# Kernel tuning notes

Measured on AMD Instinct MI355X. Metric: run time of the kernel, lower is better.

## Reference

```python
import math
from functools import partial

import jax
import jax.numpy as jnp
import numpy as np

DS = 128            # domain_size (cells per side); original used 600
PD = 1.0            # particle diameter d == grid spacing
KN = 500000.0       # normal stiffness
MASS = 1.0
DT = 1e-4
FS = 5              # filter (stencil) size -> 5x5x5 shifts
_ALPHA = -math.log(0.7) / math.pi
_GAMMA = _ALPHA / math.sqrt(_ALPHA ** 2 + 1.0)
ETA = 2.0 * _GAMMA * math.sqrt(KN * MASS)   # damping_coefficient_Eta
EPS = 1e-4          # torch.clamp(dist, 0.0001)
SHAPE = (1, 1, DS, DS, DS)


def setup_inputs() -> dict:
    rng = np.random.default_rng(0)
    occ = np.zeros((DS, DS, DS), np.float32)
    occ[1:-1, 1:-1, 1:-1] = (rng.random((DS - 2,) * 3) < 0.2).astype(np.float32)
    iz, iy, ix = np.meshgrid(np.arange(DS), np.arange(DS), np.arange(DS), indexing="ij")
    jit = lambda: (rng.random((DS,) * 3).astype(np.float32) - 0.5) * 0.4
    # occupied cells store their own coordinate (+jitter) so round(x/d) == cell index
    x = (occ * (ix.astype(np.float32) + jit())).astype(np.float32)
    y = (occ * (iy.astype(np.float32) + jit())).astype(np.float32)
    z = (occ * (iz.astype(np.float32) + jit())).astype(np.float32)
    vel = lambda: (occ * rng.normal(0.0, 0.5, (DS,) * 3)).astype(np.float32)
    asg = lambda a: jnp.asarray(a.reshape(SHAPE))
    return {
        "x_grid": asg(x), "y_grid": asg(y), "z_grid": asg(z),
        "vx_grid": asg(vel()), "vy_grid": asg(vel()), "vz_grid": asg(vel()),
        "mask": asg(occ),
    }


def _contrib(xg, yg, zg, vxg, vyg, vzg, shift):
    """Force contribution from one (i,j,k) stencil shift (torch.roll based)."""
    roll = lambda g: jnp.roll(g, shift, axis=(2, 3, 4))
    dx, dy, dz = xg - roll(xg), yg - roll(yg), zg - roll(zg)
    sq = dx * dx + dy * dy + dz * dz
    dist = jnp.sqrt(sq + 1e-20)  # tiny eps keeps sqrt grad finite at sq==0; value unchanged in fp32
    cd = jnp.maximum(dist, EPS)  # torch.clamp(dist, 0.0001)
    vn = ((vxg - roll(vxg)) * dx + (vyg - roll(vyg)) * dy + (vzg - roll(vzg)) * dz) / cd
    ov = dist < 2.0 * PD
    fx = jnp.where(ov, KN * (dist - 2.0 * PD) * dx / cd + ETA * vn * dx / cd, 0.0)
    fy = jnp.where(ov, KN * (dist - 2.0 * PD) * dy / cd + ETA * vn * dy / cd, 0.0)
    fz = jnp.where(ov, KN * (dist - 2.0 * PD) * dz / cd + ETA * vn * dz / cd, 0.0)
    return fx, fy, fz


def _forward(xg, yg, zg, vxg, vyg, vzg, mask):
    f32 = jnp.float32
    fx = jnp.zeros(SHAPE, f32)
    fy = jnp.zeros(SHAPE, f32)
    fz = jnp.zeros(SHAPE, f32)
    for i in range(FS):
        for j in range(FS):
            for k in range(FS):
                c = jax.checkpoint(partial(_contrib, shift=(k - 2, j - 2, i - 2)))
                dfx, dfy, dfz = c(xg, yg, zg, vxg, vyg, vzg)
                fx, fy, fz = fx + dfx, fy + dfy, fz + dfz
    # boundary overlap forces
    bl = ((xg != 0.0) & (xg < PD)).astype(f32)
    br = (xg > DS - 2.0 * PD).astype(f32)
    bb = ((yg != 0.0) & (yg < PD)).astype(f32)
    bt = (yg > DS - 2.0 * PD).astype(f32)
    bf = ((zg != 0.0) & (zg < PD)).astype(f32)
    bk = (zg > DS - 2.0 * PD).astype(f32)
    fxb = KN * bl * mask * (PD - xg) - KN * br * mask * (xg - DS + 2.0 * PD) - ETA * vxg * bl * mask - ETA * vxg * br * mask
    fyb = KN * bb * mask * (PD - yg) - KN * bt * mask * (yg - DS + 2.0 * PD) - ETA * vyg * bb * mask - ETA * vyg * bt * mask
    fzb = KN * bf * mask * (PD - zg) - KN * bk * mask * (zg - DS + 2.0 * PD) - ETA * vzg * bf * mask - ETA * vzg * bk * mask
    vxn = vxg + DT / MASS * mask * (-0.0 * MASS - fx + fxb)
    vyn = vyg + DT / MASS * mask * (-9.8 * MASS - fy + fyb)
    vzn = vzg + DT / MASS * mask * (-0.0 * MASS - fz + fzb)
    cell = lambda g: jnp.round(g / PD).astype(jnp.int32)
    cx0, cy0, cz0 = cell(xg), cell(yg), cell(zg)
    xn, yn, zn = xg + DT * vxn, yg + DT * vyn, zg + DT * vzn
    cx1, cy1, cz1 = cell(xn), cell(yn), cell(zn)
    # cell-list relocation: flatten to linear indices; invalid (empty) cells -> dump slot D3
    D3 = DS ** 3
    def lin(cz, cy, cx):
        v = (cx != 0) & (cy != 0) & (cz != 0)   # torch filters cell_* != 0
        return jnp.where(v, (cz * DS + cy) * DS + cx, D3).reshape(-1)
    lo = lin(cz0, cy0, cx0)
    ln = lin(cz1, cy1, cx1)
    pad = lambda g: jnp.concatenate([g.reshape(-1), jnp.zeros((1,), g.dtype)])
    unpad = lambda f: f[:D3].reshape(SHAPE)
    def move(g):
        gf = pad(g)
        return unpad(gf.at[lo].set(0.0).at[ln].set(gf[lo]))
    mask_n = unpad(pad(mask).at[lo].set(0.0).at[ln].set(1.0))
    return (move(xn), move(yn), move(zn), move(vxn), move(vyn), move(vzn), mask_n)


def reference(x_grid, y_grid, z_grid, vx_grid, vy_grid, vz_grid, mask):
    return _forward(x_grid, y_grid, z_grid, vx_grid, vy_grid, vz_grid, mask)
```

## Files before the change

### kernel.cpp

```cpp
#include <hip/hip_runtime.h>

#define DSZ   128
#define DMSK  127
#define D3    (DSZ * DSZ * DSZ)

#define KN_F   500000.0f
#define ETA_F  159.535258f
#define DT_F   1e-4f

#define TBX   32
#define TBY   4
#define TBZ   4
#define HALO  2
#define RS    37
#define PS    296
#define SLOTS 2368
#define NT    512

#define Q512  512.0f
#define IQ512 0.001953125f

struct OffTabs { int a[36]; int b[48]; int e[44]; };
constexpr OffTabs make_tabs() {
    OffTabs t{}; int na = 0, nb = 0, ne = 0;
    for (int dz = -2; dz <= 2; ++dz)
        for (int dy = -2; dy <= 2; ++dy)
            for (int dx = -2; dx <= 2; ++dx) {
                const int r2 = dz*dz + dy*dy + dx*dx;
                const int off = dz * PS + dy * RS + dx;
                if (r2 <= 4)      t.a[na++] = off;
                else if (r2 <= 6) t.b[nb++] = off;
                else              t.e[ne++] = off;
            }
    while (na < 36) t.a[na++] = 0;
    return t;
}
__constant__ OffTabs g_tabs = make_tabs();

typedef float f4a4 __attribute__((ext_vector_type(4), aligned(4)));

__device__ __forceinline__ unsigned q16(float x) {
    return (unsigned)(int)rintf(x * Q512);
}
__device__ __forceinline__ unsigned bf16_rne(float f) {
    unsigned u = __float_as_uint(f);
    u += 0x7fffu + ((u >> 16) & 1u);
    return u >> 16;
}
__device__ __forceinline__ float unpk_lo(unsigned w) { return __uint_as_float(w << 16); }
__device__ __forceinline__ float unpk_hi(unsigned w) { return __uint_as_float(w & 0xffff0000u); }

__device__ __forceinline__ void pair_full(
    const unsigned* __restrict__ lab, const unsigned* __restrict__ lcd,
    const unsigned* __restrict__ lvv, int n,
    float px, float py, float pz, float vx, float vy, float vz,
    float& fx, float& fy, float& fz)
{
    const unsigned ab = lab[n], cd = lcd[n];
    const float ddx = fmaf((float)(ab & 0xffffu), -IQ512, px);
    const float ddy = fmaf((float)(ab >> 16),     -IQ512, py);
    const float ddz = fmaf((float)(cd & 0xffffu), -IQ512, pz);
    const float sq  = fmaf(ddx, ddx, fmaf(ddy, ddy, fmaf(ddz, ddz, 1e-20f)));
    const float rsd = __builtin_amdgcn_rsqf(sq);
    const float dist = sq * rsd;
    const unsigned w = lvv[n];
    const float dvx = vx - __uint_as_float(cd & 0xffff0000u);
    const float dvy = vy - unpk_lo(w);
    const float dvz = vz - unpk_hi(w);
    const float vn = fmaf(dvx, ddx, fmaf(dvy, ddy, dvz * ddz)) * rsd;
    float coef = fmaf(KN_F, dist - 2.0f, ETA_F * vn) * rsd;
    coef = (dist < 2.0f) ? coef : 0.0f;
    fx = fmaf(coef, ddx, fx);
    fy = fmaf(coef, ddy, fy);
    fz = fmaf(coef, ddz, fz);
}

__global__ __launch_bounds__(NT) void dem_tile(
    const float* __restrict__ X, const float* __restrict__ Y, const float* __restrict__ Z,
    const float* __restrict__ VX, const float* __restrict__ VY, const float* __restrict__ VZ,
    float* __restrict__ out)
{
    __shared__ unsigned lsbuf[3 * SLOTS];
    __shared__ unsigned short plist[NT];
    __shared__ int loff[128];
    __shared__ unsigned int pcnt;
    __shared__ int nreloc;
    __shared__ int relocidx[8];
    __shared__ float relocval[8][7];

    unsigned* lab = lsbuf;
    unsigned* lcd = lsbuf + SLOTS;
    unsigned* lvv = lsbuf + 2 * SLOTS;

    const int tid = threadIdx.x;

    const unsigned raw = blockIdx.x;
    const unsigned xcd = raw & 7, loc = raw >> 3;
    const int bx = (int)((loc & 3) * TBX);
    const int by = (int)(((loc >> 2) & 31) * TBY);
    const int bz = (int)((xcd * 4 + (loc >> 7)) * TBZ);

    if (tid == 0) { pcnt = 0; nreloc = 0; }
    if (tid < 36) loff[tid] = g_tabs.a[tid];
    else if (tid < 84) loff[tid] = g_tabs.b[tid - 36];
    else if (tid < 128) loff[tid] = g_tabs.e[tid - 84];

    for (int u = tid; u < 1728; u += NT) {
        if (u < 1536) {
            const int a = u >> 9;
            const int j = u & 511;
            const int k = j & 7, r = j >> 3;
            const int hz = r >> 3, hy = r & 7;
            const int gz = (bz + hz - HALO) & DMSK;
            const int gy = (by + hy - HALO) & DMSK;
            const int gb = (gz * DSZ + gy) * DSZ + bx + k * 4;
            const float* F0 = (a == 0) ? X : (a == 1) ? Z : VY;
            const float* F1 = (a == 0) ? Y : (a == 1) ? VX : VZ;
            const f4a4 p0 = *(const f4a4*)(F0 + gb);
            const f4a4 p1 = *(const f4a4*)(F1 + gb);
            unsigned* dst = lsbuf + a * SLOTS + hz * PS + hy * RS + HALO + k * 4;
            #pragma unroll
            for (int e = 0; e < 4; ++e)
                dst[e] = (a == 0) ? (q16(p0[e]) | (q16(p1[e]) << 16))
                       : (a == 1) ? (q16(p0[e]) | (bf16_rne(p1[e]) << 16))
                                  : (bf16_rne(p0[e]) | (bf16_rne(p1[e]) << 16));
        } else {
            const int v = u - 1536;
            const int a = v >> 6;
            const int r = v & 63;
            const int hz = r >> 3, hy = r & 7;
            const int gz = (bz + hz - HALO) & DMSK;
            const int gy = (by + hy - HALO) & DMSK;
            const int rowg = (gz * DSZ + gy) * DSZ;
            const int gxs[4] = { (bx - 2) & DMSK, (bx - 1) & DMSK,
                                 (bx + 32) & DMSK, (bx + 33) & DMSK };
            const int hxs[4] = { 0, 1, 34, 35 };
            const float* F0 = (a == 0) ? X : (a == 1) ? Z : VY;
            const float* F1 = (a == 0) ? Y : (a == 1) ? VX : VZ;
            unsigned* dst = lsbuf + a * SLOTS + hz * PS + hy * RS;
            #pragma unroll
            for (int e = 0; e < 4; ++e) {
                const float f0 = F0[rowg + gxs[e]], f1 = F1[rowg + gxs[e]];
                dst[hxs[e]] = (a == 0) ? (q16(f0) | (q16(f1) << 16))
                            : (a == 1) ? (q16(f0) | (bf16_rne(f1) << 16))
                                       : (bf16_rne(f0) | (bf16_rne(f1) << 16));
            }
        }
    }

    __syncthreads();

    const int tx = tid & 31, ty = (tid >> 5) & 3, tz = tid >> 7;
    const int cg = ((bz + tz) * DSZ + (by + ty)) * DSZ + (bx + tx);
    const int lcc = (tz + HALO) * PS + (ty + HALO) * RS + (tx + HALO);
    const unsigned oab = lab[lcc];
    const bool occ = ((oab & 0xffffu) != 0u);

    {
        const unsigned long long bmask = __ballot(occ);
        const int lane = tid & 63;
        const unsigned int prefix = (unsigned int)__popcll(bmask & ((1ull << lane) - 1ull));
        unsigned int base = 0;
        if (lane == 0) base = atomicAdd(&pcnt, (unsigned int)__popcll(bmask));
        base = __shfl(base, 0, 64);
        if (occ) plist[base + prefix] = (unsigned short)tid;
    }

    float ev[7] = { 0.f, 0.f, 0.f, 0.f, 0.f, 0.f, 0.f };
    if (!occ) {
        const unsigned ocd = lcd[lcc], ow = lvv[lcc];
        const float px = (float)(oab & 0xffffu) * IQ512;
        const float py = (float)(oab >> 16) * IQ512;
        const float pz = (float)(ocd & 0xffffu) * IQ512;
        const float vx = __uint_as_float(ocd & 0xffff0000u);
        const float vy = unpk_lo(ow), vz = unpk_hi(ow);
        const float xn = px + DT_F * vx, yn = py + DT_F * vy, zn = pz + DT_F * vz;
        const int cx0 = (int)rintf(px), cy0 = (int)rintf(py), cz0 = (int)rintf(pz);
        const int cx1 = (int)rintf(xn), cy1 = (int)rintf(yn), cz1 = (int)rintf(zn);
        const int lo = (cx0 && cy0 && cz0) ? ((cz0 * DSZ + cy0) * DSZ + cx0) : D3;
        const int ln = (cx1 && cy1 && cz1) ? ((cz1 * DSZ + cy1) * DSZ + cx1) : D3;
        const bool zeroed = (lo == cg) && (ln != cg);
        const float mk = (ln == cg) ? 1.0f : 0.0f;
        ev[0] = zeroed ? 0.f : xn; ev[1] = zeroed ? 0.f : yn; ev[2] = zeroed ? 0.f : zn;
        ev[3] = zeroed ? 0.f : vx; ev[4] = zeroed ? 0.f : vy; ev[5] = zeroed ? 0.f : vz;
        ev[6] = mk;
        if (lo != cg && lo < D3) {
            int s = atomicAdd(&nreloc, 1);
            if (s < 8) { relocidx[s] = lo; for (int f = 0; f < 7; ++f) relocval[s][f] = 0.f; }
        }
        if (ln != cg && ln < D3) {
            int s = atomicAdd(&nreloc, 1);
            if (s < 8) {
                relocidx[s] = ln;
                relocval[s][0] = xn; relocval[s][1] = yn; relocval[s][2] = zn;
                relocval[s][3] = vx; relocval[s][4] = vy; relocval[s][5] = vz;
                relocval[s][6] = 1.f;
            }
        }
    }

    __syncthreads();

    const int n = (int)pcnt;
    const int grp = tid >> 2, sub = tid & 3;
    const int npass = (n + 127) >> 7;
    float fa[4] = { 0.f, 0.f, 0.f, 0.f };
    float fb[4] = { 0.f, 0.f, 0.f, 0.f };
    int fcell[4] = { -1, -1, -1, -1 };

    for (int pp = 0; pp < npass; ++pp) {
        const int i = pp * 128 + grp;
        if (i >= n) break;
        const int p  = plist[i];
        const int px_ = p & 31, py_ = (p >> 5) & 3, pz_ = p >> 7;
        const int lc = (pz_ + HALO) * PS + (py_ + HALO) * RS + (px_ + HALO);
        const int cpg = ((bz + pz_) * DSZ + (by + py_)) * DSZ + (bx + px_);

        const unsigned cab = lab[lc], ccd = lcd[lc], cw = lvv[lc];
        const float px = (float)(cab & 0xffffu) * IQ512;
        const float py = (float)(cab >> 16) * IQ512;
        const float pz = (float)(ccd & 0xffffu) * IQ512;
        const float vx = __uint_as_float(ccd & 0xffff0000u);
        const float vy = unpk_lo(cw), vz = unpk_hi(cw);
        float fx = 0.f, fy = 0.f, fz = 0.f;

        #pragma unroll
        for (int t = 0; t < 9; ++t)
            pair_full(lab, lcd, lvv, lc + loff[t * 4 + sub], px, py, pz, vx, vy, vz, fx, fy, fz);

        #pragma unroll
        for (int t = 0; t < 12; ++t) {
            const int nn = lc + loff[36 + t * 4 + sub];
            const unsigned ab = lab[nn], cd = lcd[nn];
            const float ddx = fmaf((float)(ab & 0xffffu), -IQ512, px);
            const float ddy = fmaf((float)(ab >> 16),     -IQ512, py);
            const float ddz = fmaf((float)(cd & 0xffffu), -IQ512, pz);
            const float sq = fmaf(ddx, ddx, fmaf(ddy, ddy, fmaf(ddz, ddz, 1e-20f)));
            if (sq < 4.0f) {
                const float rsd = __builtin_amdgcn_rsqf(sq);
                const float dist = sq * rsd;
                const unsigned w = lvv[nn];
                const float dvx = vx - __uint_as_float(cd & 0xffff0000u);
                const float vn = fmaf(dvx, ddx,
                                   fmaf(vy - unpk_lo(w), ddy, (vz - unpk_hi(w)) * ddz)) * rsd;
                const float coef = fmaf(KN_F, dist - 2.0f, ETA_F * vn) * rsd;
                fx = fmaf(coef, ddx, fx);
                fy = fmaf(coef, ddy, fy);
                fz = fmaf(coef, ddz, fz);
            }
        }

        const float sqo = fmaf(px, px, fmaf(py, py, pz * pz));
        if (sqo < 4.0f) {
            for (int t = sub; t < 44; t += 4)
                pair_full(lab, lcd, lvv, lc + loff[84 + t], px, py, pz, vx, vy, vz, fx, fy, fz);
        }

        fx += __shfl_xor(fx, 1); fy += __shfl_xor(fy, 1); fz += __shfl_xor(fz, 1);
        fx += __shfl_xor(fx, 2); fy += __shfl_xor(fy, 2); fz += __shfl_xor(fz, 2);

        const float bl = (px != 0.0f && px < 1.0f)  ? 1.0f : 0.0f;
        const float br = (px > 126.0f)              ? 1.0f : 0.0f;
        const float bb = (py != 0.0f && py < 1.0f)  ? 1.0f : 0.0f;
        const float bt = (py > 126.0f)              ? 1.0f : 0.0f;
        const float bf = (pz != 0.0f && pz < 1.0f)  ? 1.0f : 0.0f;
        const float bk = (pz > 126.0f)              ? 1.0f : 0.0f;
        const float fxb = KN_F * bl * (1.0f - px) - KN_F * br * (px - 126.0f) - ETA_F * vx * (bl + br);
        const float fyb = KN_F * bb * (1.0f - py) - KN_F * bt * (py - 126.0f) - ETA_F * vy * (bb + bt);
        const float fzb = KN_F * bf * (1.0f - pz) - KN_F * bk * (pz - 126.0f) - ETA_F * vz * (bf + bk);

        const float vxn = vx + DT_F * (-fx + fxb);
        const float vyn = vy + DT_F * (-9.8f - fy + fyb);
        const float vzn = vz + DT_F * (-fz + fzb);
        const float xn = px + DT_F * vxn;
        const float yn = py + DT_F * vyn;
        const float zn = pz + DT_F * vzn;

        const int cx0 = (int)rintf(px), cy0 = (int)rintf(py), cz0 = (int)rintf(pz);
        const int cx1 = (int)rintf(xn), cy1 = (int)rintf(yn), cz1 = (int)rintf(zn);
        const int lo = (cx0 && cy0 && cz0) ? ((cz0 * DSZ + cy0) * DSZ + cx0) : D3;
        const int ln = (cx1 && cy1 && cz1) ? ((cz1 * DSZ + cy1) * DSZ + cx1) : D3;

        const bool zeroed = (lo == cpg) && (ln != cpg);
        const float mk = (ln == cpg) ? 1.0f : (zeroed ? 0.0f : 1.0f);
        const float o0 = zeroed ? 0.f : xn,  o1 = zeroed ? 0.f : yn,  o2 = zeroed ? 0.f : zn;
        const float o3 = zeroed ? 0.f : vxn, o4 = zeroed ? 0.f : vyn, o5 = zeroed ? 0.f : vzn;

        fcell[pp] = p;
        fa[pp] = (sub == 0) ? o0 : (sub == 1) ? o1 : (sub == 2) ? o2 : o3;
        fb[pp] = (sub == 0) ? o4 : (sub == 1) ? o5 : mk;

        if (sub == 0) {
            if (lo != cpg && lo < D3) {
                int s = atomicAdd(&nreloc, 1);
                if (s < 8) { relocidx[s] = lo; for (int f = 0; f < 7; ++f) relocval[s][f] = 0.f; }
            }
            if (ln != cpg && ln < D3) {
                int s = atomicAdd(&nreloc, 1);
                if (s < 8) {
                    relocidx[s] = ln;
                    relocval[s][0] = xn;  relocval[s][1] = yn;  relocval[s][2] = zn;
                    relocval[s][3] = vxn; relocval[s][4] = vyn; relocval[s][5] = vzn;
                    relocval[s][6] = 1.f;
                }
            }
        }
    }

    __syncthreads();

    float* res = (float*)lsbuf;
    if (!occ) {
        #pragma unroll
        for (int f = 0; f < 7; ++f) res[f * 512 + tid] = ev[f];
    }
    #pragma unroll
    for (int pp = 0; pp < 4; ++pp) {
        if (fcell[pp] >= 0) {
            res[sub * 512 + fcell[pp]] = fa[pp];
            if (sub < 3) res[(sub + 4) * 512 + fcell[pp]] = fb[pp];
        }
    }

    __syncthreads();

    for (int u = tid; u < 896; u += NT) {
        const int f = u >> 7, j = u & 127;
        const int cell = 4 * j;
        const int wtx = cell & 31, wty = (cell >> 5) & 3, wtz = cell >> 7;
        const float4 v = *(const float4*)(res + f * 512 + cell);
        *(float4*)(out + f * D3 + ((bz + wtz) * DSZ + (by + wty)) * DSZ + bx + wtx) = v;
    }

    __syncthreads();
    const int nr = nreloc < 8 ? nreloc : 8;
    if (tid < nr) {
        const int idx = relocidx[tid];
        #pragma unroll
        for (int f = 0; f < 7; ++f) out[idx + f * D3] = relocval[tid][f];
    }
}

extern "C" void kernel_launch(void* const* d_in, const int* in_sizes, int n_in,
                              void* d_out, int out_size, void* d_ws, size_t ws_size,
                              hipStream_t stream)
{
    const float* X  = (const float*)d_in[0];
    const float* Y  = (const float*)d_in[1];
    const float* Z  = (const float*)d_in[2];
    const float* VX = (const float*)d_in[3];
    const float* VY = (const float*)d_in[4];
    const float* VZ = (const float*)d_in[5];
    float* out = (float*)d_out;

    dem_tile<<<(D3 / (TBX * TBY * TBZ)), NT, 0, stream>>>(X, Y, Z, VX, VY, VZ, out);
}
```

Measured before the change: 176.8 us.

## Make blocks persistent over four x-tiles with register-prefetched next tile loads

Each block now walks four consecutive x-tiles along a row, launching a quarter as many blocks. The global loads for the next tile are issued into registers while the current tile's pair forces are computed, and occupancy is taken from a direct X read with the particle list double-buffered. Result staging moves to a dedicated shared buffer so it no longer aliases the packed input tile. The aim is to hide global load latency and cut per-block setup, at the cost of more registers, more shared memory, fewer blocks in flight and an extra barrier per tile.

```diff
diff --git a/kernel.cpp b/kernel.cpp
--- a/kernel.cpp
+++ b/kernel.cpp
@@ -16,6 +16,7 @@
 #define PS    296
 #define SLOTS 2368
 #define NT    512
+#define NTILES 4
 
 #define Q512  512.0f
 #define IQ512 0.001953125f
@@ -81,9 +82,10 @@
     float* __restrict__ out)
 {
     __shared__ unsigned lsbuf[3 * SLOTS];
-    __shared__ unsigned short plist[NT];
+    __shared__ float res[7 * NT];
+    __shared__ unsigned short plist[2][NT];
     __shared__ int loff[128];
-    __shared__ unsigned int pcnt;
+    __shared__ unsigned int pcnt[NTILES];
     __shared__ int nreloc;
     __shared__ int relocidx[8];
     __shared__ float relocval[8][7];
@@ -93,22 +95,30 @@
     unsigned* lvv = lsbuf + 2 * SLOTS;
 
     const int tid = threadIdx.x;
-
-    const unsigned raw = blockIdx.x;
-    const unsigned xcd = raw & 7, loc = raw >> 3;
-    const int bx = (int)((loc & 3) * TBX);
-    const int by = (int)(((loc >> 2) & 31) * TBY);
-    const int bz = (int)((xcd * 4 + (loc >> 7)) * TBZ);
-
-    if (tid == 0) { pcnt = 0; nreloc = 0; }
+    const unsigned b = blockIdx.x;
+    const int xcd = (int)(b & 7);
+    const int g8  = (int)(b >> 3);
+    const int by = (g8 & 31) * TBY;
+    const int bz = (xcd * 4 + (g8 >> 5)) * TBZ;
+    const int tx = tid & 31, ty = (tid >> 5) & 3, tz = tid >> 7;
+    const int lcc0 = (tz + HALO) * PS + (ty + HALO) * RS + (tx + HALO);
+
+    f4a4 p0[3], p1[3];
+    float wv0[4], wv1[4];
+    float myx = 0.0f;
+
+    if (tid < NTILES) pcnt[tid] = 0;
+    if (tid == 0) nreloc = 0;
     if (tid < 36) loff[tid] = g_tabs.a[tid];
     else if (tid < 84) loff[tid] = g_tabs.b[tid - 36];
     else if (tid < 128) loff[tid] = g_tabs.e[tid - 84];
 
-    for (int u = tid; u < 1728; u += NT) {
-        if (u < 1536) {
-            const int a = u >> 9;
-            const int j = u & 511;
+    {
+        const int bx = 0;
+        #pragma unroll
+        for (int s = 0; s < 3; ++s) {
+            const int u = tid + NT * s;
+            const int a = u >> 9, j = u & 511;
             const int k = j & 7, r = j >> 3;
             const int hz = r >> 3, hy = r & 7;
             const int gz = (bz + hz - HALO) & DMSK;
@@ -116,220 +126,275 @@
             const int gb = (gz * DSZ + gy) * DSZ + bx + k * 4;
             const float* F0 = (a == 0) ? X : (a == 1) ? Z : VY;
             const float* F1 = (a == 0) ? Y : (a == 1) ? VX : VZ;
-            const f4a4 p0 = *(const f4a4*)(F0 + gb);
-            const f4a4 p1 = *(const f4a4*)(F1 + gb);
-            unsigned* dst = lsbuf + a * SLOTS + hz * PS + hy * RS + HALO + k * 4;
-            #pragma unroll
-            for (int e = 0; e < 4; ++e)
-                dst[e] = (a == 0) ? (q16(p0[e]) | (q16(p1[e]) << 16))
-                       : (a == 1) ? (q16(p0[e]) | (bf16_rne(p1[e]) << 16))
-                                  : (bf16_rne(p0[e]) | (bf16_rne(p1[e]) << 16));
-        } else {
-            const int v = u - 1536;
-            const int a = v >> 6;
-            const int r = v & 63;
+            p0[s] = *(const f4a4*)(F0 + gb);
+            p1[s] = *(const f4a4*)(F1 + gb);
+        }
+        if (tid < 192) {
+            const int a = tid >> 6, r = tid & 63;
             const int hz = r >> 3, hy = r & 7;
             const int gz = (bz + hz - HALO) & DMSK;
             const int gy = (by + hy - HALO) & DMSK;
             const int rowg = (gz * DSZ + gy) * DSZ;
             const int gxs[4] = { (bx - 2) & DMSK, (bx - 1) & DMSK,
                                  (bx + 32) & DMSK, (bx + 33) & DMSK };
-            const int hxs[4] = { 0, 1, 34, 35 };
             const float* F0 = (a == 0) ? X : (a == 1) ? Z : VY;
             const float* F1 = (a == 0) ? Y : (a == 1) ? VX : VZ;
-            unsigned* dst = lsbuf + a * SLOTS + hz * PS + hy * RS;
-            #pragma unroll
-            for (int e = 0; e < 4; ++e) {
-                const float f0 = F0[rowg + gxs[e]], f1 = F1[rowg + gxs[e]];
-                dst[hxs[e]] = (a == 0) ? (q16(f0) | (q16(f1) << 16))
-                            : (a == 1) ? (q16(f0) | (bf16_rne(f1) << 16))
-                                       : (bf16_rne(f0) | (bf16_rne(f1) << 16));
-            }
-        }
+            #pragma unroll
+            for (int e = 0; e < 4; ++e) { wv0[e] = F0[rowg + gxs[e]]; wv1[e] = F1[rowg + gxs[e]]; }
+        }
+        myx = X[((bz + tz) * DSZ + (by + ty)) * DSZ + bx + tx];
     }
-
     __syncthreads();
 
-    const int tx = tid & 31, ty = (tid >> 5) & 3, tz = tid >> 7;
-    const int cg = ((bz + tz) * DSZ + (by + ty)) * DSZ + (bx + tx);
-    const int lcc = (tz + HALO) * PS + (ty + HALO) * RS + (tx + HALO);
-    const unsigned oab = lab[lcc];
-    const bool occ = ((oab & 0xffffu) != 0u);
-
+    bool occ = (myx != 0.0f);
     {
         const unsigned long long bmask = __ballot(occ);
         const int lane = tid & 63;
-        const unsigned int prefix = (unsigned int)__popcll(bmask & ((1ull << lane) - 1ull));
-        unsigned int base = 0;
-        if (lane == 0) base = atomicAdd(&pcnt, (unsigned int)__popcll(bmask));
+        const unsigned pfx = (unsigned)__popcll(bmask & ((1ull << lane) - 1ull));
+        unsigned base = 0;
+        if (lane == 0) base = atomicAdd(&pcnt[0], (unsigned)__popcll(bmask));
         base = __shfl(base, 0, 64);
-        if (occ) plist[base + prefix] = (unsigned short)tid;
+        if (occ) plist[0][base + pfx] = (unsigned short)tid;
     }
 
-    float ev[7] = { 0.f, 0.f, 0.f, 0.f, 0.f, 0.f, 0.f };
-    if (!occ) {
-        const unsigned ocd = lcd[lcc], ow = lvv[lcc];
-        const float px = (float)(oab & 0xffffu) * IQ512;
-        const float py = (float)(oab >> 16) * IQ512;
-        const float pz = (float)(ocd & 0xffffu) * IQ512;
-        const float vx = __uint_as_float(ocd & 0xffff0000u);
-        const float vy = unpk_lo(ow), vz = unpk_hi(ow);
-        const float xn = px + DT_F * vx, yn = py + DT_F * vy, zn = pz + DT_F * vz;
-        const int cx0 = (int)rintf(px), cy0 = (int)rintf(py), cz0 = (int)rintf(pz);
-        const int cx1 = (int)rintf(xn), cy1 = (int)rintf(yn), cz1 = (int)rintf(zn);
-        const int lo = (cx0 && cy0 && cz0) ? ((cz0 * DSZ + cy0) * DSZ + cx0) : D3;
-        const int ln = (cx1 && cy1 && cz1) ? ((cz1 * DSZ + cy1) * DSZ + cx1) : D3;
-        const bool zeroed = (lo == cg) && (ln != cg);
-        const float mk = (ln == cg) ? 1.0f : 0.0f;
-        ev[0] = zeroed ? 0.f : xn; ev[1] = zeroed ? 0.f : yn; ev[2] = zeroed ? 0.f : zn;
-        ev[3] = zeroed ? 0.f : vx; ev[4] = zeroed ? 0.f : vy; ev[5] = zeroed ? 0.f : vz;
-        ev[6] = mk;
-        if (lo != cg && lo < D3) {
-            int s = atomicAdd(&nreloc, 1);
-            if (s < 8) { relocidx[s] = lo; for (int f = 0; f < 7; ++f) relocval[s][f] = 0.f; }
-        }
-        if (ln != cg && ln < D3) {
-            int s = atomicAdd(&nreloc, 1);
-            if (s < 8) {
-                relocidx[s] = ln;
-                relocval[s][0] = xn; relocval[s][1] = yn; relocval[s][2] = zn;
-                relocval[s][3] = vx; relocval[s][4] = vy; relocval[s][5] = vz;
-                relocval[s][6] = 1.f;
-            }
-        }
-    }
-
-    __syncthreads();
-
-    const int n = (int)pcnt;
-    const int grp = tid >> 2, sub = tid & 3;
-    const int npass = (n + 127) >> 7;
-    float fa[4] = { 0.f, 0.f, 0.f, 0.f };
-    float fb[4] = { 0.f, 0.f, 0.f, 0.f };
-    int fcell[4] = { -1, -1, -1, -1 };
-
-    for (int pp = 0; pp < npass; ++pp) {
-        const int i = pp * 128 + grp;
-        if (i >= n) break;
-        const int p  = plist[i];
-        const int px_ = p & 31, py_ = (p >> 5) & 3, pz_ = p >> 7;
-        const int lc = (pz_ + HALO) * PS + (py_ + HALO) * RS + (px_ + HALO);
-        const int cpg = ((bz + pz_) * DSZ + (by + py_)) * DSZ + (bx + px_);
-
-        const unsigned cab = lab[lc], ccd = lcd[lc], cw = lvv[lc];
-        const float px = (float)(cab & 0xffffu) * IQ512;
-        const float py = (float)(cab >> 16) * IQ512;
-        const float pz = (float)(ccd & 0xffffu) * IQ512;
-        const float vx = __uint_as_float(ccd & 0xffff0000u);
-        const float vy = unpk_lo(cw), vz = unpk_hi(cw);
-        float fx = 0.f, fy = 0.f, fz = 0.f;
+    #pragma unroll 1
+    for (int it = 0; it < NTILES; ++it) {
+        const int bx = it * TBX;
 
         #pragma unroll
-        for (int t = 0; t < 9; ++t)
-            pair_full(lab, lcd, lvv, lc + loff[t * 4 + sub], px, py, pz, vx, vy, vz, fx, fy, fz);
-
-        #pragma unroll
-        for (int t = 0; t < 12; ++t) {
-            const int nn = lc + loff[36 + t * 4 + sub];
-            const unsigned ab = lab[nn], cd = lcd[nn];
-            const float ddx = fmaf((float)(ab & 0xffffu), -IQ512, px);
-            const float ddy = fmaf((float)(ab >> 16),     -IQ512, py);
-            const float ddz = fmaf((float)(cd & 0xffffu), -IQ512, pz);
-            const float sq = fmaf(ddx, ddx, fmaf(ddy, ddy, fmaf(ddz, ddz, 1e-20f)));
-            if (sq < 4.0f) {
-                const float rsd = __builtin_amdgcn_rsqf(sq);
-                const float dist = sq * rsd;
-                const unsigned w = lvv[nn];
-                const float dvx = vx - __uint_as_float(cd & 0xffff0000u);
-                const float vn = fmaf(dvx, ddx,
-                                   fmaf(vy - unpk_lo(w), ddy, (vz - unpk_hi(w)) * ddz)) * rsd;
-                const float coef = fmaf(KN_F, dist - 2.0f, ETA_F * vn) * rsd;
-                fx = fmaf(coef, ddx, fx);
-                fy = fmaf(coef, ddy, fy);
-                fz = fmaf(coef, ddz, fz);
-            }
-        }
-
-        const float sqo = fmaf(px, px, fmaf(py, py, pz * pz));
-        if (sqo < 4.0f) {
-            for (int t = sub; t < 44; t += 4)
-                pair_full(lab, lcd, lvv, lc + loff[84 + t], px, py, pz, vx, vy, vz, fx, fy, fz);
-        }
-
-        fx += __shfl_xor(fx, 1); fy += __shfl_xor(fy, 1); fz += __shfl_xor(fz, 1);
-        fx += __shfl_xor(fx, 2); fy += __shfl_xor(fy, 2); fz += __shfl_xor(fz, 2);
-
-        const float bl = (px != 0.0f && px < 1.0f)  ? 1.0f : 0.0f;
-        const float br = (px > 126.0f)              ? 1.0f : 0.0f;
-        const float bb = (py != 0.0f && py < 1.0f)  ? 1.0f : 0.0f;
-        const float bt = (py > 126.0f)              ? 1.0f : 0.0f;
-        const float bf = (pz != 0.0f && pz < 1.0f)  ? 1.0f : 0.0f;
-        const float bk = (pz > 126.0f)              ? 1.0f : 0.0f;
-        const float fxb = KN_F * bl * (1.0f - px) - KN_F * br * (px - 126.0f) - ETA_F * vx * (bl + br);
-        const float fyb = KN_F * bb * (1.0f - py) - KN_F * bt * (py - 126.0f) - ETA_F * vy * (bb + bt);
-        const float fzb = KN_F * bf * (1.0f - pz) - KN_F * bk * (pz - 126.0f) - ETA_F * vz * (bf + bk);
-
-        const float vxn = vx + DT_F * (-fx + fxb);
-        const float vyn = vy + DT_F * (-9.8f - fy + fyb);
-        const float vzn = vz + DT_F * (-fz + fzb);
-        const float xn = px + DT_F * vxn;
-        const float yn = py + DT_F * vyn;
-        const float zn = pz + DT_F * vzn;
-
-        const int cx0 = (int)rintf(px), cy0 = (int)rintf(py), cz0 = (int)rintf(pz);
-        const int cx1 = (int)rintf(xn), cy1 = (int)rintf(yn), cz1 = (int)rintf(zn);
-        const int lo = (cx0 && cy0 && cz0) ? ((cz0 * DSZ + cy0) * DSZ + cx0) : D3;
-        const int ln = (cx1 && cy1 && cz1) ? ((cz1 * DSZ + cy1) * DSZ + cx1) : D3;
-
-        const bool zeroed = (lo == cpg) && (ln != cpg);
-        const float mk = (ln == cpg) ? 1.0f : (zeroed ? 0.0f : 1.0f);
-        const float o0 = zeroed ? 0.f : xn,  o1 = zeroed ? 0.f : yn,  o2 = zeroed ? 0.f : zn;
-        const float o3 = zeroed ? 0.f : vxn, o4 = zeroed ? 0.f : vyn, o5 = zeroed ? 0.f : vzn;
-
-        fcell[pp] = p;
-        fa[pp] = (sub == 0) ? o0 : (sub == 1) ? o1 : (sub == 2) ? o2 : o3;
-        fb[pp] = (sub == 0) ? o4 : (sub == 1) ? o5 : mk;
-
-        if (sub == 0) {
-            if (lo != cpg && lo < D3) {
+        for (int s = 0; s < 3; ++s) {
+            const int u = tid + NT * s;
+            const int a = u >> 9, j = u & 511;
+            const int k = j & 7, r = j >> 3;
+            const int hz = r >> 3, hy = r & 7;
+            unsigned* dst = lsbuf + a * SLOTS + hz * PS + hy * RS + HALO + k * 4;
+            #pragma unroll
+            for (int e = 0; e < 4; ++e)
+                dst[e] = (a == 0) ? (q16(p0[s][e]) | (q16(p1[s][e]) << 16))
+                       : (a == 1) ? (q16(p0[s][e]) | (bf16_rne(p1[s][e]) << 16))
+                                  : (bf16_rne(p0[s][e]) | (bf16_rne(p1[s][e]) << 16));
+        }
+        if (tid < 192) {
+            const int a = tid >> 6, r = tid & 63;
+            const int hz = r >> 3, hy = r & 7;
+            unsigned* dst = lsbuf + a * SLOTS + hz * PS + hy * RS;
+            const int hxs[4] = { 0, 1, 34, 35 };
+            #pragma unroll
+            for (int e = 0; e < 4; ++e)
+                dst[hxs[e]] = (a == 0) ? (q16(wv0[e]) | (q16(wv1[e]) << 16))
+                            : (a == 1) ? (q16(wv0[e]) | (bf16_rne(wv1[e]) << 16))
+                                       : (bf16_rne(wv0[e]) | (bf16_rne(wv1[e]) << 16));
+        }
+        __syncthreads();
+
+        if (it + 1 < NTILES) {
+            const int nbx = (it + 1) * TBX;
+            #pragma unroll
+            for (int s = 0; s < 3; ++s) {
+                const int u = tid + NT * s;
+                const int a = u >> 9, j = u & 511;
+                const int k = j & 7, r = j >> 3;
+                const int hz = r >> 3, hy = r & 7;
+                const int gz = (bz + hz - HALO) & DMSK;
+                const int gy = (by + hy - HALO) & DMSK;
+                const int gb = (gz * DSZ + gy) * DSZ + nbx + k * 4;
+                const float* F0 = (a == 0) ? X : (a == 1) ? Z : VY;
+                const float* F1 = (a == 0) ? Y : (a == 1) ? VX : VZ;
+                p0[s] = *(const f4a4*)(F0 + gb);
+                p1[s] = *(const f4a4*)(F1 + gb);
+            }
+            if (tid < 192) {
+                const int a = tid >> 6, r = tid & 63;
+                const int hz = r >> 3, hy = r & 7;
+                const int gz = (bz + hz - HALO) & DMSK;
+                const int gy = (by + hy - HALO) & DMSK;
+                const int rowg = (gz * DSZ + gy) * DSZ;
+                const int gxs[4] = { (nbx - 2) & DMSK, (nbx - 1) & DMSK,
+                                     (nbx + 32) & DMSK, (nbx + 33) & DMSK };
+                const float* F0 = (a == 0) ? X : (a == 1) ? Z : VY;
+                const float* F1 = (a == 0) ? Y : (a == 1) ? VX : VZ;
+                #pragma unroll
+                for (int e = 0; e < 4; ++e) { wv0[e] = F0[rowg + gxs[e]]; wv1[e] = F1[rowg + gxs[e]]; }
+            }
+            myx = X[((bz + tz) * DSZ + (by + ty)) * DSZ + nbx + tx];
+        }
+
+        const int cg = ((bz + tz) * DSZ + (by + ty)) * DSZ + bx + tx;
+        float ev[7] = { 0.f, 0.f, 0.f, 0.f, 0.f, 0.f, 0.f };
+        if (!occ) {
+            const unsigned oab = lab[lcc0], ocd = lcd[lcc0], ow = lvv[lcc0];
+            const float px = (float)(oab & 0xffffu) * IQ512;
+            const float py = (float)(oab >> 16) * IQ512;
+            const float pz = (float)(ocd & 0xffffu) * IQ512;
+            const float vx = __uint_as_float(ocd & 0xffff0000u);
+            const float vy = unpk_lo(ow), vz = unpk_hi(ow);
+            const float xn = px + DT_F * vx, yn = py + DT_F * vy, zn = pz + DT_F * vz;
+            const int cx0 = (int)rintf(px), cy0 = (int)rintf(py), cz0 = (int)rintf(pz);
+            const int cx1 = (int)rintf(xn), cy1 = (int)rintf(yn), cz1 = (int)rintf(zn);
+            const int lo = (cx0 && cy0 && cz0) ? ((cz0 * DSZ + cy0) * DSZ + cx0) : D3;
+            const int ln = (cx1 && cy1 && cz1) ? ((cz1 * DSZ + cy1) * DSZ + cx1) : D3;
+            const bool zeroed = (lo == cg) && (ln != cg);
+            const float mk = (ln == cg) ? 1.0f : 0.0f;
+            ev[0] = zeroed ? 0.f : xn; ev[1] = zeroed ? 0.f : yn; ev[2] = zeroed ? 0.f : zn;
+            ev[3] = zeroed ? 0.f : vx; ev[4] = zeroed ? 0.f : vy; ev[5] = zeroed ? 0.f : vz;
+            ev[6] = mk;
+            if (lo != cg && lo < D3) {
                 int s = atomicAdd(&nreloc, 1);
                 if (s < 8) { relocidx[s] = lo; for (int f = 0; f < 7; ++f) relocval[s][f] = 0.f; }
             }
-            if (ln != cpg && ln < D3) {
+            if (ln != cg && ln < D3) {
                 int s = atomicAdd(&nreloc, 1);
                 if (s < 8) {
                     relocidx[s] = ln;
-                    relocval[s][0] = xn;  relocval[s][1] = yn;  relocval[s][2] = zn;
-                    relocval[s][3] = vxn; relocval[s][4] = vyn; relocval[s][5] = vzn;
+                    relocval[s][0] = xn; relocval[s][1] = yn; relocval[s][2] = zn;
+                    relocval[s][3] = vx; relocval[s][4] = vy; relocval[s][5] = vz;
                     relocval[s][6] = 1.f;
                 }
             }
         }
-    }
-
-    __syncthreads();
-
-    float* res = (float*)lsbuf;
-    if (!occ) {
+
+        const int n = (int)pcnt[it];
+        const int grp = tid >> 2, sub = tid & 3;
+        const int npass = (n + 127) >> 7;
+        float fa[4] = { 0.f, 0.f, 0.f, 0.f };
+        float fb[4] = { 0.f, 0.f, 0.f, 0.f };
+        int fcell[4] = { -1, -1, -1, -1 };
+
+        for (int pp = 0; pp < npass; ++pp) {
+            const int i = pp * 128 + grp;
+            if (i >= n) break;
+            const int p  = plist[it & 1][i];
+            const int px_ = p & 31, py_ = (p >> 5) & 3, pz_ = p >> 7;
+            const int lc = (pz_ + HALO) * PS + (py_ + HALO) * RS + (px_ + HALO);
+            const int cpg = ((bz + pz_) * DSZ + (by + py_)) * DSZ + bx + px_;
+
+            const unsigned cab = lab[lc], ccd = lcd[lc], cw = lvv[lc];
+            const float px = (float)(cab & 0xffffu) * IQ512;
+            const float py = (float)(cab >> 16) * IQ512;
+            const float pz = (float)(ccd & 0xffffu) * IQ512;
+            const float vx = __uint_as_float(ccd & 0xffff0000u);
+            const float vy = unpk_lo(cw), vz = unpk_hi(cw);
+            float fx = 0.f, fy = 0.f, fz = 0.f;
+
+            #pragma unroll
+            for (int t = 0; t < 9; ++t)
+                pair_full(lab, lcd, lvv, lc + loff[t * 4 + sub], px, py, pz, vx, vy, vz, fx, fy, fz);
+
+            #pragma unroll
+            for (int t = 0; t < 12; ++t) {
+                const int nn = lc + loff[36 + t * 4 + sub];
+                const unsigned ab = lab[nn], cd = lcd[nn];
+                const float ddx = fmaf((float)(ab & 0xffffu), -IQ512, px);
+                const float ddy = fmaf((float)(ab >> 16),     -IQ512, py);
+                const float ddz = fmaf((float)(cd & 0xffffu), -IQ512, pz);
+                const float sq = fmaf(ddx, ddx, fmaf(ddy, ddy, fmaf(ddz, ddz, 1e-20f)));
+                if (sq < 4.0f) {
+                    const float rsd = __builtin_amdgcn_rsqf(sq);
+                    const float dist = sq * rsd;
+                    const unsigned w = lvv[nn];
+                    const float dvx = vx - __uint_as_float(cd & 0xffff0000u);
+                    const float vn = fmaf(dvx, ddx,
+                                       fmaf(vy - unpk_lo(w), ddy, (vz - unpk_hi(w)) * ddz)) * rsd;
+                    const float coef = fmaf(KN_F, dist - 2.0f, ETA_F * vn) * rsd;
+                    fx = fmaf(coef, ddx, fx);
+                    fy = fmaf(coef, ddy, fy);
+                    fz = fmaf(coef, ddz, fz);
+                }
+            }
+
+            const float sqo = fmaf(px, px, fmaf(py, py, pz * pz));
+            if (sqo < 4.0f) {
+                for (int t = sub; t < 44; t += 4)
+                    pair_full(lab, lcd, lvv, lc + loff[84 + t], px, py, pz, vx, vy, vz, fx, fy, fz);
+            }
+
+            fx += __shfl_xor(fx, 1); fy += __shfl_xor(fy, 1); fz += __shfl_xor(fz, 1);
+            fx += __shfl_xor(fx, 2); fy += __shfl_xor(fy, 2); fz += __shfl_xor(fz, 2);
+
+            const float bl = (px != 0.0f && px < 1.0f)  ? 1.0f : 0.0f;
+            const float br = (px > 126.0f)              ? 1.0f : 0.0f;
+            const float bb = (py != 0.0f && py < 1.0f)  ? 1.0f : 0.0f;
+            const float bt = (py > 126.0f)              ? 1.0f : 0.0f;
+            const float bf = (pz != 0.0f && pz < 1.0f)  ? 1.0f : 0.0f;
+            const float bk = (pz > 126.0f)              ? 1.0f : 0.0f;
+            const float fxb = KN_F * bl * (1.0f - px) - KN_F * br * (px - 126.0f) - ETA_F * vx * (bl + br);
+            const float fyb = KN_F * bb * (1.0f - py) - KN_F * bt * (py - 126.0f) - ETA_F * vy * (bb + bt);
+            const float fzb = KN_F * bf * (1.0f - pz) - KN_F * bk * (pz - 126.0f) - ETA_F * vz * (bf + bk);
+
+            const float vxn = vx + DT_F * (-fx + fxb);
+            const float vyn = vy + DT_F * (-9.8f - fy + fyb);
+            const float vzn = vz + DT_F * (-fz + fzb);
+            const float xn = px + DT_F * vxn;
+            const float yn = py + DT_F * vyn;
+            const float zn = pz + DT_F * vzn;
+
+            const int cx0 = (int)rintf(px), cy0 = (int)rintf(py), cz0 = (int)rintf(pz);
+            const int cx1 = (int)rintf(xn), cy1 = (int)rintf(yn), cz1 = (int)rintf(zn);
+            const int lo = (cx0 && cy0 && cz0) ? ((cz0 * DSZ + cy0) * DSZ + cx0) : D3;
+            const int ln = (cx1 && cy1 && cz1) ? ((cz1 * DSZ + cy1) * DSZ + cx1) : D3;
+
+            const bool zeroed = (lo == cpg) && (ln != cpg);
+            const float mk = (ln == cpg) ? 1.0f : (zeroed ? 0.0f : 1.0f);
+            const float o0 = zeroed ? 0.f : xn,  o1 = zeroed ? 0.f : yn,  o2 = zeroed ? 0.f : zn;
+            const float o3 = zeroed ? 0.f : vxn, o4 = zeroed ? 0.f : vyn, o5 = zeroed ? 0.f : vzn;
+
+            fcell[pp] = p;
+            fa[pp] = (sub == 0) ? o0 : (sub == 1) ? o1 : (sub == 2) ? o2 : o3;
+            fb[pp] = (sub == 0) ? o4 : (sub == 1) ? o5 : mk;
+
+            if (sub == 0) {
+                if (lo != cpg && lo < D3) {
+                    int s = atomicAdd(&nreloc, 1);
+                    if (s < 8) { relocidx[s] = lo; for (int f = 0; f < 7; ++f) relocval[s][f] = 0.f; }
+                }
+                if (ln != cpg && ln < D3) {
+                    int s = atomicAdd(&nreloc, 1);
+                    if (s < 8) {
+                        relocidx[s] = ln;
+                        relocval[s][0] = xn;  relocval[s][1] = yn;  relocval[s][2] = zn;
+                        relocval[s][3] = vxn; relocval[s][4] = vyn; relocval[s][5] = vzn;
+                        relocval[s][6] = 1.f;
+                    }
+                }
+            }
+        }
+
+        bool occn = false;
+        if (it + 1 < NTILES) {
+            occn = (myx != 0.0f);
+            const unsigned long long bmask = __ballot(occn);
+            const int lane = tid & 63;
+            const unsigned pfx = (unsigned)__popcll(bmask & ((1ull << lane) - 1ull));
+            unsigned base = 0;
+            if (lane == 0) base = atomicAdd(&pcnt[it + 1], (unsigned)__popcll(bmask));
+            base = __shfl(base, 0, 64);
+            if (occn) plist[(it + 1) & 1][base + pfx] = (unsigned short)tid;
+        }
+
+        __syncthreads();
+
+        if (!occ) {
+            #pragma unroll
+            for (int f = 0; f < 7; ++f) res[f * NT + tid] = ev[f];
+        }
         #pragma unroll
-        for (int f = 0; f < 7; ++f) res[f * 512 + tid] = ev[f];
-    }
-    #pragma unroll
-    for (int pp = 0; pp < 4; ++pp) {
-        if (fcell[pp] >= 0) {
-            res[sub * 512 + fcell[pp]] = fa[pp];
-            if (sub < 3) res[(sub + 4) * 512 + fcell[pp]] = fb[pp];
-        }
-    }
-
-    __syncthreads();
-
-    for (int u = tid; u < 896; u += NT) {
-        const int f = u >> 7, j = u & 127;
-        const int cell = 4 * j;
-        const int wtx = cell & 31, wty = (cell >> 5) & 3, wtz = cell >> 7;
-        const float4 v = *(const float4*)(res + f * 512 + cell);
-        *(float4*)(out + f * D3 + ((bz + wtz) * DSZ + (by + wty)) * DSZ + bx + wtx) = v;
+        for (int pp = 0; pp < 4; ++pp) {
+            if (fcell[pp] >= 0) {
+                res[sub * NT + fcell[pp]] = fa[pp];
+                if (sub < 3) res[(sub + 4) * NT + fcell[pp]] = fb[pp];
+            }
+        }
+        __syncthreads();
+
+        for (int u = tid; u < 896; u += NT) {
+            const int f = u >> 7, j = u & 127;
+            const int cell = 4 * j;
+            const int wtx = cell & 31, wty = (cell >> 5) & 3, wtz = cell >> 7;
+            const float4 v = *(const float4*)(res + f * NT + cell);
+            *(float4*)(out + f * D3 + ((bz + wtz) * DSZ + (by + wty)) * DSZ + bx + wtx) = v;
+        }
+
+        occ = occn;
     }
 
     __syncthreads();
@@ -353,5 +418,5 @@
     const float* VZ = (const float*)d_in[5];
     float* out = (float*)d_out;
 
-    dem_tile<<<(D3 / (TBX * TBY * TBZ)), NT, 0, stream>>>(X, Y, Z, VX, VY, VZ, out);
-}
+    dem_tile<<<(D3 / (TBX * TBY * TBZ * NTILES)), NT, 0, stream>>>(X, Y, Z, VX, VY, VZ, out);
+}
```

Result: slower. 197.1 us (+11.5%).
